# Kernel tuning notes

Measured on AMD Instinct MI355X. Metric: run time of the kernel, lower is better.

The kernel has to match this reference:

```python
import jax, jax.numpy as jnp
import numpy as np

HEADS = 8
DIM_HEAD = 64
SCALE = DIM_HEAD ** -0.5

def setup_inputs() -> dict:
    key = jax.random.key(0)
    ks = jax.random.split(key, 6)
    b, n, m, qd, cd = 4, 2048, 2048, 256, 256
    inner = HEADS * DIM_HEAD
    return {
        "x": jax.random.normal(ks[0], (b, n, qd), jnp.float32),
        "context": jax.random.normal(ks[1], (b, m, cd), jnp.float32),
        "Wq": jax.random.normal(ks[2], (inner, qd), jnp.float32) * 0.02,
        "bq": jnp.zeros((inner,), jnp.float32),
        "Wkv": jax.random.normal(ks[3], (2 * inner, cd), jnp.float32) * 0.02,
        "bkv": jnp.zeros((2 * inner,), jnp.float32),
        "Wo": jax.random.normal(ks[4], (qd, inner), jnp.float32) * 0.02,
        "bo": jnp.zeros((qd,), jnp.float32),
    }

def reference(x, context, Wq, bq, Wkv, bkv, Wo, bo):
    b, n, _ = x.shape
    m = context.shape[1]
    inner = HEADS * DIM_HEAD
    # 1x1 conv projections == pointwise linear
    q = jnp.einsum('bnd,ed->bne', x, Wq) + bq            # [b, n, inner]
    kv = jnp.einsum('bmd,ed->bme', context, Wkv) + bkv    # [b, m, 2*inner]
    k, v = kv[..., :inner], kv[..., inner:]
    q = q.reshape(b, n, HEADS, DIM_HEAD).transpose(0, 2, 1, 3)  # [b,h,n,d]
    k = k.reshape(b, m, HEADS, DIM_HEAD).transpose(0, 2, 1, 3)
    v = v.reshape(b, m, HEADS, DIM_HEAD).transpose(0, 2, 1, 3)
    sim = jnp.einsum('bhid,bhjd->bhij', q, k) * SCALE     # [b,h,n,m]
    attn = jax.nn.softmax(sim, axis=-1)
    out = jnp.einsum('bhij,bhjd->bhid', attn, v)          # [b,h,n,d]
    out = out.transpose(0, 2, 1, 3).reshape(b, n, inner)  # [b,n,inner]
    return jnp.einsum('bne,oe->bno', out, Wo) + bo        # [b,n,query_dim]
```

## Files before the change

kernel.cpp:

```cpp
#include <hip/hip_runtime.h>
#include <hip/hip_bf16.h>

#define NB 4
#define SEQ 2048
#define NHEADS 8
#define ROWS (NB * SEQ)

typedef __attribute__((ext_vector_type(8))) short bf16x8;
typedef __attribute__((ext_vector_type(4))) short bf16x4;
typedef __attribute__((ext_vector_type(4))) float f32x4;
typedef __attribute__((ext_vector_type(16))) float f32x16;

__device__ inline short f2bf(float x) {
    union { float f; unsigned u; } v; v.f = x;
    unsigned r = v.u + 0x7FFF + ((v.u >> 16) & 1);
    return (short)(r >> 16);
}

__device__ inline unsigned pack2bf(float a, float b) {
    __hip_bfloat162 h = __float22bfloat162_rn(make_float2(a, b));
    unsigned u; __builtin_memcpy(&u, &h, 4);
    return u;
}

__device__ inline unsigned comb2(unsigned w1, unsigned w2, float inv) {
    union { unsigned v; float f; } a, b, c, d;
    a.v = w1 << 16;          b.v = w2 << 16;
    c.v = w1 & 0xffff0000u;  d.v = w2 & 0xffff0000u;
    return pack2bf((a.f + b.f) * inv, (c.f + d.f) * inv);
}

__global__ __launch_bounds__(256) void cvt_all(
    const float* __restrict__ x, const float* __restrict__ ctx,
    const float* __restrict__ wq, const float* __restrict__ wkv,
    const float* __restrict__ wo,
    short* __restrict__ xb, short* __restrict__ cb, short* __restrict__ wqb,
    short* __restrict__ wkvb, short* __restrict__ wob)
{
    const int i = blockIdx.x * 256 + threadIdx.x;
    const float* src; short* dst; int off;
    if (i < 524288)       { src = x;   dst = xb;   off = i; }
    else if (i < 1048576) { src = ctx; dst = cb;   off = i - 524288; }
    else if (i < 1081344) { src = wq;  dst = wqb;  off = i - 1048576; }
    else if (i < 1146880) { src = wkv; dst = wkvb; off = i - 1081344; }
    else                  { src = wo;  dst = wob;  off = i - 1146880; }
    const float4 v = ((const float4*)src)[off];
    uint2 o2;
    o2.x = pack2bf(v.x, v.y);
    o2.y = pack2bf(v.z, v.w);
    *(uint2*)(dst + (size_t)off * 4) = o2;
}

__global__ __launch_bounds__(256, 3) void proj2(
    const short* __restrict__ xb, const short* __restrict__ wqb,
    const float* __restrict__ bq,
    const short* __restrict__ cb, const short* __restrict__ wkvb,
    const float* __restrict__ bkv,
    short* __restrict__ q2b, short* __restrict__ kv2b, float qscale)
{
    __shared__ short As[128 * 64];
    __shared__ short Ws[128 * 64];
    const int tid = threadIdx.x;
    const int bid = blockIdx.x;
    const int w = tid >> 6, lane = tid & 63, low = lane & 15, quad = lane >> 4;
    const int wm = w >> 1, wn = w & 1;
    const int K = 256;

    const short* A; const short* W; const float* bias;
    short* outp; int Ccols; float scale; int rM0, c0;
    if (bid < 512) {
        A = cb; W = wkvb; bias = bkv; outp = kv2b; Ccols = 1024; scale = 1.0f;
        c0 = (bid & 7) * 128; rM0 = (bid >> 3) * 128;
    } else {
        const int u = bid - 512;
        A = xb; W = wqb; bias = bq; outp = q2b; Ccols = 512; scale = qscale;
        c0 = (u & 3) * 128; rM0 = (u >> 2) * 128;
    }

    const int srow = tid >> 3, sj = tid & 7;

    f32x4 acc[4][4];
#pragma unroll
    for (int mt = 0; mt < 4; ++mt)
#pragma unroll
        for (int nt = 0; nt < 4; ++nt) acc[mt][nt] = (f32x4){0.f, 0.f, 0.f, 0.f};

    bf16x8 pab[4], pwb[4];
#pragma unroll
    for (int c = 0; c < 4; ++c) {
        const int row = c * 32 + srow;
        pab[c] = *(const bf16x8*)(A + (size_t)(rM0 + row) * K + sj * 8);
        pwb[c] = *(const bf16x8*)(W + (size_t)(c0 + row) * K + sj * 8);
    }

    int k0 = 0;
    for (;;) {
        __syncthreads();
#pragma unroll
        for (int c = 0; c < 4; ++c) {
            const int row = c * 32 + srow;
            const int pc = sj ^ (row & 7);
            *(bf16x8*)(&As[row * 64 + pc * 8]) = pab[c];
            *(bf16x8*)(&Ws[row * 64 + pc * 8]) = pwb[c];
        }
        __syncthreads();
        const int kn = k0 + 64;
        if (kn < K) {
#pragma unroll
            for (int c = 0; c < 4; ++c) {
                const int row = c * 32 + srow;
                pab[c] = *(const bf16x8*)(A + (size_t)(rM0 + row) * K + kn + sj * 8);
                pwb[c] = *(const bf16x8*)(W + (size_t)(c0 + row) * K + kn + sj * 8);
            }
        }
#pragma unroll
        for (int kh = 0; kh < 2; ++kh) {
            bf16x8 af[4], bfv[4];
#pragma unroll
            for (int t = 0; t < 4; ++t) {
                const int ra = wm * 64 + t * 16 + low;
                af[t] = *(const bf16x8*)(&As[ra * 64 + ((kh * 4 + quad) ^ (ra & 7)) * 8]);
                const int rb = wn * 64 + t * 16 + low;
                bfv[t] = *(const bf16x8*)(&Ws[rb * 64 + ((kh * 4 + quad) ^ (rb & 7)) * 8]);
            }
#pragma unroll
            for (int mt = 0; mt < 4; ++mt)
#pragma unroll
                for (int nt = 0; nt < 4; ++nt)
                    acc[mt][nt] = __builtin_amdgcn_mfma_f32_16x16x32_bf16(af[mt], bfv[nt], acc[mt][nt], 0, 0, 0);
        }
        k0 = kn;
        if (k0 >= K) break;
    }

#pragma unroll
    for (int nt = 0; nt < 4; ++nt) {
        const int col = c0 + wn * 64 + nt * 16 + low;
        const float bv = bias[col];
#pragma unroll
        for (int mt = 0; mt < 4; ++mt) {
            const size_t rbase = (size_t)(rM0 + wm * 64 + mt * 16 + quad * 4);
#pragma unroll
            for (int r = 0; r < 4; ++r)
                outp[(rbase + r) * Ccols + col] = f2bf((acc[mt][nt][r] + bv) * scale);
        }
    }
}

__global__ __launch_bounds__(256) void gemm64_ocomb(
    const short* __restrict__ num, const float* __restrict__ lbuf,
    const short* __restrict__ W, const float* __restrict__ bias,
    float* __restrict__ out)
{
    const int K = 512, Ccols = 256;
    const size_t NHALF = (size_t)ROWS * 512;
    const int R8 = ROWS * 8;
    __shared__ short As[64 * 64];
    __shared__ short Ws[64 * 64];
    const int tid = threadIdx.x;
    const int w = tid >> 6, lane = tid & 63, low = lane & 15, quad = lane >> 4;
    const int wm = w >> 1, wn = w & 1;
    const int r0 = blockIdx.y * 64, c0 = blockIdx.x * 64;
    const int srow = tid >> 2;
    const int sc = (tid & 3) * 2;

    f32x4 acc[2][2];
#pragma unroll
    for (int mt = 0; mt < 2; ++mt)
#pragma unroll
        for (int nt = 0; nt < 2; ++nt) acc[mt][nt] = (f32x4){0.f, 0.f, 0.f, 0.f};

    uint4 pa1[2], pa2[2];
    float pinv;
    bf16x8 pwb[2];

    auto loadA = [&](int k0) {
        const int hh = k0 >> 6;
        const int row = r0 + srow;
        pinv = lbuf[row * 8 + hh] + lbuf[R8 + row * 8 + hh];
        const short* p1 = num + (size_t)row * 512 + k0 + sc * 8;
        pa1[0] = ((const uint4*)p1)[0];
        pa1[1] = ((const uint4*)p1)[1];
        const short* p2 = p1 + NHALF;
        pa2[0] = ((const uint4*)p2)[0];
        pa2[1] = ((const uint4*)p2)[1];
    };
    auto loadW = [&](int k0) {
        const short* p = W + (size_t)(c0 + srow) * K + k0 + sc * 8;
        pwb[0] = ((const bf16x8*)p)[0];
        pwb[1] = ((const bf16x8*)p)[1];
    };

    loadA(0); loadW(0);

    int k0 = 0;
    for (;;) {
        __syncthreads();
        {
            const float inv = 1.f / pinv;
#pragma unroll
            for (int c = 0; c < 2; ++c) {
                const int pc = (sc + c) ^ (srow & 7);
                union { unsigned u[4]; bf16x8 v; } r;
                r.u[0] = comb2(pa1[c].x, pa2[c].x, inv);
                r.u[1] = comb2(pa1[c].y, pa2[c].y, inv);
                r.u[2] = comb2(pa1[c].z, pa2[c].z, inv);
                r.u[3] = comb2(pa1[c].w, pa2[c].w, inv);
                *(bf16x8*)(&As[srow * 64 + pc * 8]) = r.v;
                *(bf16x8*)(&Ws[srow * 64 + pc * 8]) = pwb[c];
            }
        }
        __syncthreads();
        const int kn = k0 + 64;
        if (kn < K) { loadA(kn); loadW(kn); }
#pragma unroll
        for (int kh = 0; kh < 2; ++kh) {
            bf16x8 af[2], bfv[2];
#pragma unroll
            for (int t = 0; t < 2; ++t) {
                const int ra = wm * 32 + t * 16 + low;
                af[t] = *(const bf16x8*)(&As[ra * 64 + ((kh * 4 + quad) ^ (ra & 7)) * 8]);
                const int rb = wn * 32 + t * 16 + low;
                bfv[t] = *(const bf16x8*)(&Ws[rb * 64 + ((kh * 4 + quad) ^ (rb & 7)) * 8]);
            }
#pragma unroll
            for (int mt = 0; mt < 2; ++mt)
#pragma unroll
                for (int nt = 0; nt < 2; ++nt)
                    acc[mt][nt] = __builtin_amdgcn_mfma_f32_16x16x32_bf16(af[mt], bfv[nt], acc[mt][nt], 0, 0, 0);
        }
        k0 = kn;
        if (k0 >= K) break;
    }

#pragma unroll
    for (int nt = 0; nt < 2; ++nt) {
        const int col = c0 + wn * 32 + nt * 16 + low;
        const float bv = bias[col];
#pragma unroll
        for (int mt = 0; mt < 2; ++mt) {
            const size_t rbase = (size_t)(r0 + wm * 32 + mt * 16 + quad * 4);
#pragma unroll
            for (int r = 0; r < 4; ++r)
                out[(rbase + r) * Ccols + col] = acc[mt][nt][r] + bv;
        }
    }
}

#define KST 72
#define VST 72
#define PST 72

__global__ __launch_bounds__(256) void attn_mfma(
    const short* __restrict__ q2,
    const short* __restrict__ kv2,
    short* __restrict__ numb,
    float* __restrict__ lbuf)
{
    __shared__ short Ks[64 * KST];
    __shared__ short Vt[64 * VST];
    __shared__ short Ps[4][32 * PST];

    const int tid = threadIdx.x;
    const int w = tid >> 6;
    const int lane = tid & 63;
    const int l31 = lane & 31;
    const int h2 = lane >> 5;

    const int flat = blockIdx.x;
    const int h = flat & 7;
    const int rest = flat >> 3;
    const int half = rest & 1;
    const int rest2 = rest >> 1;
    const int qtile = rest2 & 15;
    const int b = rest2 >> 4;
    const int iq0 = qtile * 128;
    const int jt0 = half * 16;

    bf16x8 qr[4];
#pragma unroll
    for (int st = 0; st < 4; ++st)
        qr[st] = *(const bf16x8*)(q2 + (size_t)(b * SEQ + iq0 + w * 32 + l31) * 512
                                  + h * 64 + st * 16 + h2 * 8);

    const short* kbase = kv2 + (size_t)(b * SEQ) * 1024 + h * 64;
    const short* vbase = kbase + 512;
    short* pw = &Ps[w][0];

    float lsum = 0.f;
    f32x16 oacc[2];
#pragma unroll
    for (int dg = 0; dg < 2; ++dg)
#pragma unroll
        for (int r = 0; r < 16; ++r) oacc[dg][r] = 0.f;

    const int krow = tid >> 2;
    const int kc = (tid & 3) * 16;
    const int vk4 = (tid & 15) * 4;
    const int vd4 = (tid >> 4) * 4;

    bf16x8 pk0, pk1;
    bf16x4 pv0, pv1, pv2, pv3;
    {
        const short* ksrc = kbase + (size_t)(jt0 * 64 + krow) * 1024 + kc;
        pk0 = *(const bf16x8*)(ksrc);
        pk1 = *(const bf16x8*)(ksrc + 8);
        const short* vs = vbase + (size_t)(jt0 * 64 + vk4) * 1024 + vd4;
        pv0 = *(const bf16x4*)(vs);
        pv1 = *(const bf16x4*)(vs + 1024);
        pv2 = *(const bf16x4*)(vs + 2048);
        pv3 = *(const bf16x4*)(vs + 3072);
    }

    for (int jt = jt0; jt < jt0 + 16; ++jt) {
        __syncthreads();
        *(bf16x8*)(&Ks[krow * KST + kc]) = pk0;
        *(bf16x8*)(&Ks[krow * KST + kc + 8]) = pk1;
        {
            bf16x4 c0_, c1_, c2_, c3_;
            c0_[0] = pv0[0]; c0_[1] = pv1[0]; c0_[2] = pv2[0]; c0_[3] = pv3[0];
            c1_[0] = pv0[1]; c1_[1] = pv1[1]; c1_[2] = pv2[1]; c1_[3] = pv3[1];
            c2_[0] = pv0[2]; c2_[1] = pv1[2]; c2_[2] = pv2[2]; c2_[3] = pv3[2];
            c3_[0] = pv0[3]; c3_[1] = pv1[3]; c3_[2] = pv2[3]; c3_[3] = pv3[3];
            *(bf16x4*)(&Vt[(vd4 + 0) * VST + vk4]) = c0_;
            *(bf16x4*)(&Vt[(vd4 + 1) * VST + vk4]) = c1_;
            *(bf16x4*)(&Vt[(vd4 + 2) * VST + vk4]) = c2_;
            *(bf16x4*)(&Vt[(vd4 + 3) * VST + vk4]) = c3_;
        }
        __syncthreads();

        if (jt + 1 < jt0 + 16) {
            const short* ksrc = kbase + (size_t)((jt + 1) * 64 + krow) * 1024 + kc;
            pk0 = *(const bf16x8*)(ksrc);
            pk1 = *(const bf16x8*)(ksrc + 8);
            const short* vs = vbase + (size_t)((jt + 1) * 64 + vk4) * 1024 + vd4;
            pv0 = *(const bf16x4*)(vs);
            pv1 = *(const bf16x4*)(vs + 1024);
            pv2 = *(const bf16x4*)(vs + 2048);
            pv3 = *(const bf16x4*)(vs + 3072);
        }

#pragma unroll
        for (int kg = 0; kg < 2; ++kg) {
            f32x16 s;
#pragma unroll
            for (int r = 0; r < 16; ++r) s[r] = 0.f;
#pragma unroll
            for (int st = 0; st < 4; ++st) {
                const bf16x8 kf = *(const bf16x8*)(&Ks[(kg * 32 + l31) * KST + st * 16 + h2 * 8]);
                s = __builtin_amdgcn_mfma_f32_32x32x16_bf16(kf, qr[st], s, 0, 0, 0);
            }
#pragma unroll
            for (int g = 0; g < 4; ++g) {
                const float p0 = __builtin_amdgcn_exp2f(s[4 * g + 0]);
                const float p1 = __builtin_amdgcn_exp2f(s[4 * g + 1]);
                const float p2 = __builtin_amdgcn_exp2f(s[4 * g + 2]);
                const float p3 = __builtin_amdgcn_exp2f(s[4 * g + 3]);
                lsum += (p0 + p1) + (p2 + p3);
                uint2 u;
                u.x = pack2bf(p0, p1);
                u.y = pack2bf(p2, p3);
                *(uint2*)(&pw[l31 * PST + kg * 32 + 8 * g + 4 * h2]) = u;
            }
        }
        __builtin_amdgcn_wave_barrier();

#pragma unroll
        for (int st = 0; st < 4; ++st) {
            const bf16x8 pf = *(const bf16x8*)(&pw[l31 * PST + st * 16 + h2 * 8]);
#pragma unroll
            for (int dg = 0; dg < 2; ++dg) {
                const bf16x8 vf = *(const bf16x8*)(&Vt[(dg * 32 + l31) * VST + st * 16 + h2 * 8]);
                oacc[dg] = __builtin_amdgcn_mfma_f32_32x32x16_bf16(pf, vf, oacc[dg], 0, 0, 0);
            }
        }
        __builtin_amdgcn_wave_barrier();
    }

    lsum += __shfl_xor(lsum, 32);
    short* nb = numb + (size_t)half * ROWS * 512;
    float* lb = lbuf + (size_t)half * ROWS * 8;
    if (lane < 32)
        lb[(size_t)(b * SEQ + iq0 + w * 32 + l31) * 8 + h] = lsum;
#pragma unroll
    for (int dg = 0; dg < 2; ++dg)
#pragma unroll
        for (int r = 0; r < 16; ++r) {
            const int qrow = w * 32 + (r & 3) + 8 * (r >> 2) + 4 * h2;
            nb[(size_t)(b * SEQ + iq0 + qrow) * 512 + h * 64 + dg * 32 + l31] =
                f2bf(oacc[dg][r]);
        }
}

extern "C" void kernel_launch(void* const* d_in, const int* in_sizes, int n_in,
                              void* d_out, int out_size, void* d_ws, size_t ws_size,
                              hipStream_t stream) {
    const float* x   = (const float*)d_in[0];
    const float* ctx = (const float*)d_in[1];
    const float* Wq  = (const float*)d_in[2];
    const float* bq  = (const float*)d_in[3];
    const float* Wkv = (const float*)d_in[4];
    const float* bkv = (const float*)d_in[5];
    const float* Wo  = (const float*)d_in[6];
    const float* bo  = (const float*)d_in[7];
    float* out = (float*)d_out;

    short* xb   = (short*)d_ws;
    short* cb   = xb + (size_t)ROWS * 256;
    short* wqb  = cb + (size_t)ROWS * 256;
    short* wkvb = wqb + 131072;
    short* wob  = wkvb + 262144;
    short* q2b  = wob + 131072;
    short* kv2b = q2b + (size_t)ROWS * 512;
    short* numb = kv2b + (size_t)ROWS * 1024;
    float* lbuf = (float*)(numb + (size_t)2 * ROWS * 512);

    const float qscale = 0.125f * 1.44269504088896f;

    cvt_all<<<4608, 256, 0, stream>>>(x, ctx, Wq, Wkv, Wo,
                                      xb, cb, wqb, wkvb, wob);
    proj2<<<768, 256, 0, stream>>>(xb, wqb, bq, cb, wkvb, bkv,
                                   q2b, kv2b, qscale);
    attn_mfma<<<NB * NHEADS * (SEQ / 128) * 2, 256, 0, stream>>>(
        q2b, kv2b, numb, lbuf);
    gemm64_ocomb<<<dim3(256 / 64, ROWS / 64), 256, 0, stream>>>(
        numb, lbuf, wob, bo, out);
}
```

Before: 162.0 us.

## Split softmax combine into separate kernel and use 128x128 output GEMM tiles

The fused combine-plus-output-projection GEMM with 64x64 tiles is replaced by a standalone elementwise combine kernel that writes normalized bf16 activations into a reused workspace (xb). A plain 128x128-tile GEMM then performs the output projection. The goal is to avoid re-reading and re-combining the two partial numerators for every column tile and to raise MFMA reuse per block. In exchange it adds one kernel launch and an extra round trip of the combined tensor through memory, and the output GEMM launches only 128 blocks. The projection kernel's block-to-tile mapping is also reordered to group row tiles together for better cache locality.

```diff
diff --git a/kernel.cpp b/kernel.cpp
--- a/kernel.cpp
+++ b/kernel.cpp
@@ -70,11 +70,13 @@
     short* outp; int Ccols; float scale; int rM0, c0;
     if (bid < 512) {
         A = cb; W = wkvb; bias = bkv; outp = kv2b; Ccols = 1024; scale = 1.0f;
-        c0 = (bid & 7) * 128; rM0 = (bid >> 3) * 128;
+        const int rlo = bid & 7, rest = bid >> 3;
+        c0 = (rest & 7) * 128; rM0 = (rlo + 8 * (rest >> 3)) * 128;
     } else {
         const int u = bid - 512;
         A = xb; W = wqb; bias = bq; outp = q2b; Ccols = 512; scale = qscale;
-        c0 = (u & 3) * 128; rM0 = (u >> 2) * 128;
+        const int rlo = u & 7, rest = u >> 3;
+        c0 = (rest & 3) * 128; rM0 = (rlo + 8 * (rest >> 2)) * 128;
     }
 
     const int srow = tid >> 3, sj = tid & 7;
@@ -147,86 +149,88 @@
     }
 }
 
-__global__ __launch_bounds__(256) void gemm64_ocomb(
+__global__ __launch_bounds__(256) void combine(
     const short* __restrict__ num, const float* __restrict__ lbuf,
-    const short* __restrict__ W, const float* __restrict__ bias,
-    float* __restrict__ out)
+    short* __restrict__ ob)
+{
+    const size_t NHALF = (size_t)ROWS * 512;
+    const int R8 = ROWS * 8;
+    const int i = blockIdx.x * 256 + threadIdx.x;
+    const size_t e0 = (size_t)i * 8;
+    const int row = (int)(e0 >> 9);
+    const int h = (int)((e0 >> 6) & 7);
+    const float inv = 1.f / (lbuf[row * 8 + h] + lbuf[R8 + row * 8 + h]);
+    const uint4 a = *(const uint4*)(num + e0);
+    const uint4 b = *(const uint4*)(num + NHALF + e0);
+    uint4 o;
+    o.x = comb2(a.x, b.x, inv);
+    o.y = comb2(a.y, b.y, inv);
+    o.z = comb2(a.z, b.z, inv);
+    o.w = comb2(a.w, b.w, inv);
+    *(uint4*)(ob + e0) = o;
+}
+
+__global__ __launch_bounds__(256, 3) void gemm128_o(
+    const short* __restrict__ A, const short* __restrict__ W,
+    const float* __restrict__ bias, float* __restrict__ out)
 {
     const int K = 512, Ccols = 256;
-    const size_t NHALF = (size_t)ROWS * 512;
-    const int R8 = ROWS * 8;
-    __shared__ short As[64 * 64];
-    __shared__ short Ws[64 * 64];
+    __shared__ short As[128 * 64];
+    __shared__ short Ws[128 * 64];
     const int tid = threadIdx.x;
     const int w = tid >> 6, lane = tid & 63, low = lane & 15, quad = lane >> 4;
     const int wm = w >> 1, wn = w & 1;
-    const int r0 = blockIdx.y * 64, c0 = blockIdx.x * 64;
-    const int srow = tid >> 2;
-    const int sc = (tid & 3) * 2;
-
-    f32x4 acc[2][2];
-#pragma unroll
-    for (int mt = 0; mt < 2; ++mt)
-#pragma unroll
-        for (int nt = 0; nt < 2; ++nt) acc[mt][nt] = (f32x4){0.f, 0.f, 0.f, 0.f};
-
-    uint4 pa1[2], pa2[2];
-    float pinv;
-    bf16x8 pwb[2];
-
-    auto loadA = [&](int k0) {
-        const int hh = k0 >> 6;
-        const int row = r0 + srow;
-        pinv = lbuf[row * 8 + hh] + lbuf[R8 + row * 8 + hh];
-        const short* p1 = num + (size_t)row * 512 + k0 + sc * 8;
-        pa1[0] = ((const uint4*)p1)[0];
-        pa1[1] = ((const uint4*)p1)[1];
-        const short* p2 = p1 + NHALF;
-        pa2[0] = ((const uint4*)p2)[0];
-        pa2[1] = ((const uint4*)p2)[1];
-    };
-    auto loadW = [&](int k0) {
-        const short* p = W + (size_t)(c0 + srow) * K + k0 + sc * 8;
-        pwb[0] = ((const bf16x8*)p)[0];
-        pwb[1] = ((const bf16x8*)p)[1];
-    };
-
-    loadA(0); loadW(0);
+    const int rM0 = blockIdx.y * 128, c0 = blockIdx.x * 128;
+    const int srow = tid >> 3, sj = tid & 7;
+
+    f32x4 acc[4][4];
+#pragma unroll
+    for (int mt = 0; mt < 4; ++mt)
+#pragma unroll
+        for (int nt = 0; nt < 4; ++nt) acc[mt][nt] = (f32x4){0.f, 0.f, 0.f, 0.f};
+
+    bf16x8 pab[4], pwb[4];
+#pragma unroll
+    for (int c = 0; c < 4; ++c) {
+        const int row = c * 32 + srow;
+        pab[c] = *(const bf16x8*)(A + (size_t)(rM0 + row) * K + sj * 8);
+        pwb[c] = *(const bf16x8*)(W + (size_t)(c0 + row) * K + sj * 8);
+    }
 
     int k0 = 0;
     for (;;) {
         __syncthreads();
-        {
-            const float inv = 1.f / pinv;
-#pragma unroll
-            for (int c = 0; c < 2; ++c) {
-                const int pc = (sc + c) ^ (srow & 7);
-                union { unsigned u[4]; bf16x8 v; } r;
-                r.u[0] = comb2(pa1[c].x, pa2[c].x, inv);
-                r.u[1] = comb2(pa1[c].y, pa2[c].y, inv);
-                r.u[2] = comb2(pa1[c].z, pa2[c].z, inv);
-                r.u[3] = comb2(pa1[c].w, pa2[c].w, inv);
-                *(bf16x8*)(&As[srow * 64 + pc * 8]) = r.v;
-                *(bf16x8*)(&Ws[srow * 64 + pc * 8]) = pwb[c];
-            }
+#pragma unroll
+        for (int c = 0; c < 4; ++c) {
+            const int row = c * 32 + srow;
+            const int pc = sj ^ (row & 7);
+            *(bf16x8*)(&As[row * 64 + pc * 8]) = pab[c];
+            *(bf16x8*)(&Ws[row * 64 + pc * 8]) = pwb[c];
         }
         __syncthreads();
         const int kn = k0 + 64;
-        if (kn < K) { loadA(kn); loadW(kn); }
+        if (kn < K) {
+#pragma unroll
+            for (int c = 0; c < 4; ++c) {
+                const int row = c * 32 + srow;
+                pab[c] = *(const bf16x8*)(A + (size_t)(rM0 + row) * K + kn + sj * 8);
+                pwb[c] = *(const bf16x8*)(W + (size_t)(c0 + row) * K + kn + sj * 8);
+            }
+        }
 #pragma unroll
         for (int kh = 0; kh < 2; ++kh) {
-            bf16x8 af[2], bfv[2];
-#pragma unroll
-            for (int t = 0; t < 2; ++t) {
-                const int ra = wm * 32 + t * 16 + low;
+            bf16x8 af[4], bfv[4];
+#pragma unroll
+            for (int t = 0; t < 4; ++t) {
+                const int ra = wm * 64 + t * 16 + low;
                 af[t] = *(const bf16x8*)(&As[ra * 64 + ((kh * 4 + quad) ^ (ra & 7)) * 8]);
-                const int rb = wn * 32 + t * 16 + low;
+                const int rb = wn * 64 + t * 16 + low;
                 bfv[t] = *(const bf16x8*)(&Ws[rb * 64 + ((kh * 4 + quad) ^ (rb & 7)) * 8]);
             }
 #pragma unroll
-            for (int mt = 0; mt < 2; ++mt)
-#pragma unroll
-                for (int nt = 0; nt < 2; ++nt)
+            for (int mt = 0; mt < 4; ++mt)
+#pragma unroll
+                for (int nt = 0; nt < 4; ++nt)
                     acc[mt][nt] = __builtin_amdgcn_mfma_f32_16x16x32_bf16(af[mt], bfv[nt], acc[mt][nt], 0, 0, 0);
         }
         k0 = kn;
@@ -234,12 +238,12 @@
     }
 
 #pragma unroll
-    for (int nt = 0; nt < 2; ++nt) {
-        const int col = c0 + wn * 32 + nt * 16 + low;
+    for (int nt = 0; nt < 4; ++nt) {
+        const int col = c0 + wn * 64 + nt * 16 + low;
         const float bv = bias[col];
 #pragma unroll
-        for (int mt = 0; mt < 2; ++mt) {
-            const size_t rbase = (size_t)(r0 + wm * 32 + mt * 16 + quad * 4);
+        for (int mt = 0; mt < 4; ++mt) {
+            const size_t rbase = (size_t)(rM0 + wm * 64 + mt * 16 + quad * 4);
 #pragma unroll
             for (int r = 0; r < 4; ++r)
                 out[(rbase + r) * Ccols + col] = acc[mt][nt][r] + bv;
@@ -414,6 +418,7 @@
     short* kv2b = q2b + (size_t)ROWS * 512;
     short* numb = kv2b + (size_t)ROWS * 1024;
     float* lbuf = (float*)(numb + (size_t)2 * ROWS * 512);
+    short* ob   = xb;
 
     const float qscale = 0.125f * 1.44269504088896f;
 
@@ -423,6 +428,6 @@
                                    q2b, kv2b, qscale);
     attn_mfma<<<NB * NHEADS * (SEQ / 128) * 2, 256, 0, stream>>>(
         q2b, kv2b, numb, lbuf);
-    gemm64_ocomb<<<dim3(256 / 64, ROWS / 64), 256, 0, stream>>>(
-        numb, lbuf, wob, bo, out);
-}
+    combine<<<ROWS * 512 / 8 / 256, 256, 0, stream>>>(numb, lbuf, ob);
+    gemm128_o<<<dim3(2, 64), 256, 0, stream>>>(ob, wob, bo, out);
+}
```

After: 165.7 us. +2.3%, slower.
